# Kernel optimization log

Measured on AMD Instinct MI355X. Metric: run time of the kernel, lower is better.

## Reference

```python
import jax, jax.numpy as jnp
import numpy as np

EMBED_DIM = 1024
NUM_HEADS = 16
HEAD_DIM = EMBED_DIM // NUM_HEADS
EPS = 1e-6
B, T = 4, 8192


def setup_inputs() -> dict:
    key = jax.random.key(0)
    ks = jax.random.split(key, 11)
    s = 1.0 / np.sqrt(EMBED_DIM)
    inp = {
        'query': jax.random.normal(ks[0], (B, T, EMBED_DIM), jnp.float32),
        'key': jax.random.normal(ks[1], (B, T, EMBED_DIM), jnp.float32),
        'value': jax.random.normal(ks[2], (B, T, EMBED_DIM), jnp.float32),
        'Wq': jax.random.normal(ks[3], (EMBED_DIM, EMBED_DIM), jnp.float32) * s,
        'bq': jnp.zeros((EMBED_DIM,), jnp.float32),
        'Wk': jax.random.normal(ks[4], (EMBED_DIM, EMBED_DIM), jnp.float32) * s,
        'bk': jnp.zeros((EMBED_DIM,), jnp.float32),
        'Wv': jax.random.normal(ks[5], (EMBED_DIM, EMBED_DIM), jnp.float32) * s,
        'bv': jnp.zeros((EMBED_DIM,), jnp.float32),
        'Wo': jax.random.normal(ks[6], (EMBED_DIM, EMBED_DIM), jnp.float32) * s,
        'bo': jnp.zeros((EMBED_DIM,), jnp.float32),
    }
    return inp


def _feature_map(x):
    return jax.nn.elu(x) + 1.0


def reference(query, key, value, Wq, bq, Wk, bk, Wv, bv, Wo, bo):
    b, t, _ = query.shape
    # projections (torch Linear: x @ W.T + b)
    q = query @ Wq.T + bq
    k = key @ Wk.T + bk
    v = value @ Wv.T + bv
    # split heads -> (b, h, t, d)
    def split(x):
        return x.reshape(b, t, NUM_HEADS, HEAD_DIM).transpose(0, 2, 1, 3)
    q = _feature_map(split(q))
    k = _feature_map(split(k))
    v = split(v)
    k_sum = k.sum(axis=2)                                   # (b,h,d)
    denom = jnp.einsum('bhtd,bhd->bht', q, k_sum) + EPS     # (b,h,t)
    kv = jnp.einsum('bhtd,bhtv->bhdv', k, v)                # (b,h,d,d)
    out = jnp.einsum('bhtd,bhde->bhte', q, kv) / denom[..., None]
    out = out.transpose(0, 2, 1, 3).reshape(b, t, EMBED_DIM)
    return out @ Wo.T + bo
```

## Files before the change

### kernel.cpp

```cpp
#include <hip/hip_runtime.h>
#include <hip/hip_bf16.h>

typedef long long TLONG;
typedef float  f32x4_t  __attribute__((ext_vector_type(4)));
typedef short  s16x8_t  __attribute__((ext_vector_type(8)));
typedef short  s16x4_t  __attribute__((ext_vector_type(4)));
typedef __bf16 bf16x8_t __attribute__((ext_vector_type(8)));

#define MDIM 32768
#define NDIM 1024
#define KDIM 1024
#define EPSV 1e-6f

#define BARRIER() asm volatile("s_barrier" ::: "memory")
#define SBAR() __builtin_amdgcn_sched_barrier(0)

__device__ __forceinline__ unsigned short f2bf_bits(float f) {
  __hip_bfloat16 h = __float2bfloat16(f);
  return __builtin_bit_cast(unsigned short, h);
}
__device__ __forceinline__ float bf2f(unsigned short u) {
  unsigned int x = ((unsigned int)u) << 16;
  return __builtin_bit_cast(float, x);
}
__device__ __forceinline__ void load_lds16(const void* g, void* l) {
  __builtin_amdgcn_global_load_lds((const __attribute__((address_space(1))) void*)g,
                                   (__attribute__((address_space(3))) void*)l, 16, 0, 0);
}

__device__ __forceinline__ void conv8(const float* __restrict__ in,
                                      unsigned short* __restrict__ out, TLONG i) {
  f32x4_t a = *reinterpret_cast<const f32x4_t*>(in + i);
  f32x4_t b = *reinterpret_cast<const f32x4_t*>(in + i + 4);
  s16x8_t o;
  o[0] = (short)f2bf_bits(a[0]); o[1] = (short)f2bf_bits(a[1]);
  o[2] = (short)f2bf_bits(a[2]); o[3] = (short)f2bf_bits(a[3]);
  o[4] = (short)f2bf_bits(b[0]); o[5] = (short)f2bf_bits(b[1]);
  o[6] = (short)f2bf_bits(b[2]); o[7] = (short)f2bf_bits(b[3]);
  *reinterpret_cast<s16x8_t*>(out + i) = o;
}

__global__ __launch_bounds__(256) void convert3_f32_bf16(
    const float* __restrict__ a, const float* __restrict__ b, const float* __restrict__ c,
    unsigned short* __restrict__ oa, unsigned short* __restrict__ ob,
    unsigned short* __restrict__ oc) {
  int blk = blockIdx.x;
  const float* in; unsigned short* out;
  if (blk < 2048)      { in = a; out = oa; }
  else if (blk < 4096) { in = b; out = ob; blk -= 2048; }
  else                 { in = c; out = oc; blk -= 4096; }
  const TLONG n = 33554432LL;
  TLONG i = ((TLONG)blk * 256 + threadIdx.x) * 8;
  const TLONG stride = 2048LL * 256 * 8;
  for (; i < n; i += stride) conv8(in, out, i);
}
__global__ __launch_bounds__(256) void convertW_f32_bf16(
    const float* __restrict__ a, const float* __restrict__ b, const float* __restrict__ c,
    const float* __restrict__ d, unsigned short* __restrict__ oa,
    unsigned short* __restrict__ ob, unsigned short* __restrict__ oc,
    unsigned short* __restrict__ od) {
  int blk = blockIdx.x;
  const float* in; unsigned short* out;
  if (blk < 512)       { in = a; out = oa; }
  else if (blk < 1024) { in = b; out = ob; blk -= 512; }
  else if (blk < 1536) { in = c; out = oc; blk -= 1024; }
  else                 { in = d; out = od; blk -= 1536; }
  TLONG i = ((TLONG)blk * 256 + threadIdx.x) * 8;
  conv8(in, out, i);
}

template <int FMAP, int OUT>
__global__ __launch_bounds__(512, 2) void gemm256(
    const unsigned short* __restrict__ A, const unsigned short* __restrict__ W,
    const float* __restrict__ bias, void* __restrict__ Cout) {
  __shared__ short lds[65536];
  const int bid = blockIdx.x;
  const int swz = (bid & 7) * 64 + (bid >> 3);
  const int mt = swz >> 2;
  const int nt = swz & 3;

  const int tid = threadIdx.x;
  const int lane = tid & 63;
  const int w = tid >> 6;
  const int wr = w >> 2, wc = w & 3;
  const int l15 = lane & 15, lh = lane >> 4;

  const int arow0 = mt * 256, brow0 = nt * 256;

  auto stage_half = [&](const unsigned short* __restrict__ src, int ldsOff,
                        int grow, int k0) {
#pragma unroll
    for (int i = 0; i < 2; ++i) {
      const int c = i * 512 + tid;
      const int r = c >> 3, ps = c & 7;
      load_lds16(src + (grow + r) * KDIM + k0 + ((ps ^ (r & 7)) * 8),
                 &lds[ldsOff + c * 8]);
    }
  };

  f32x4_t acc[8][4];
#pragma unroll
  for (int m = 0; m < 8; ++m)
#pragma unroll
    for (int n = 0; n < 4; ++n) acc[m][n] = (f32x4_t)0.0f;

  s16x8_t Af[8][2], Bf[4][2];

  auto rdA = [&](int pb, int m, int ks) -> s16x8_t {
    const int row = wr * 128 + m * 16 + l15;
    return *reinterpret_cast<const s16x8_t*>(
        &lds[pb + row * 64 + (((ks * 4 + lh) ^ (row & 7)) * 8)]);
  };
  auto rdB = [&](int pb, int n, int ks) -> s16x8_t {
    const int row = wc * 64 + n * 16 + l15;
    return *reinterpret_cast<const s16x8_t*>(
        &lds[pb + 16384 + row * 64 + (((ks * 4 + lh) ^ (row & 7)) * 8)]);
  };
  auto quad = [&](int mb, int nl) {
    __builtin_amdgcn_s_setprio(1);
#pragma unroll
    for (int m = 0; m < 4; ++m)
#pragma unroll
      for (int n = 0; n < 2; ++n)
#pragma unroll
        for (int ks = 0; ks < 2; ++ks)
          acc[mb + m][nl + n] = __builtin_amdgcn_mfma_f32_16x16x32_bf16(
              __builtin_bit_cast(bf16x8_t, Af[mb + m][ks]),
              __builtin_bit_cast(bf16x8_t, Bf[nl + n][ks]),
              acc[mb + m][nl + n], 0, 0, 0);
    __builtin_amdgcn_s_setprio(0);
  };

  stage_half(A, 0,             arow0,       0);
  stage_half(A, 8192,          arow0 + 128, 0);
  stage_half(W, 16384,         brow0,       0);
  stage_half(W, 16384 + 8192,  brow0 + 128, 0);
  stage_half(A, 32768,         arow0,       64);
  stage_half(A, 32768 + 8192,  arow0 + 128, 64);
  asm volatile("s_waitcnt vmcnt(4)" ::: "memory");
  SBAR();
  BARRIER();

  for (int kt = 0; kt < 16; ++kt) {
    const int p = kt & 1;
    const int pb = p * 32768, qb = 32768 - pb;
    const int k1 = ((kt + 1) & 15) * 64;
    const int k2 = ((kt + 2) & 15) * 64;
#pragma unroll
    for (int m = 0; m < 4; ++m)
#pragma unroll
      for (int ks = 0; ks < 2; ++ks) Af[m][ks] = rdA(pb, m, ks);
#pragma unroll
    for (int n = 0; n < 2; ++n)
#pragma unroll
      for (int ks = 0; ks < 2; ++ks) Bf[n][ks] = rdB(pb, n, ks);
    SBAR();
#pragma unroll
    for (int m = 0; m < 4; ++m)
#pragma unroll
      for (int ks = 0; ks < 2; ++ks) Af[4 + m][ks] = rdA(pb, 4 + m, ks);
    SBAR();
#pragma unroll
    for (int n = 2; n < 4; ++n)
#pragma unroll
      for (int ks = 0; ks < 2; ++ks) Bf[n][ks] = rdB(pb, n, ks);
    SBAR();
    stage_half(W, qb + 16384, brow0, k1);
    BARRIER();
    asm volatile("s_waitcnt lgkmcnt(12)" ::: "memory");
    SBAR();
    quad(0, 0);
    BARRIER();
    stage_half(W, qb + 16384 + 8192, brow0 + 128, k1);
    BARRIER();
    asm volatile("s_waitcnt lgkmcnt(4)" ::: "memory");
    SBAR();
    quad(4, 0);
    BARRIER();
    stage_half(A, pb, arow0, k2);
    BARRIER();
    asm volatile("s_waitcnt lgkmcnt(0)" ::: "memory");
    SBAR();
    quad(0, 2);
    BARRIER();
    stage_half(A, pb + 8192, arow0 + 128, k2);
    BARRIER();
    quad(4, 2);
    asm volatile("s_waitcnt vmcnt(4)" ::: "memory");
    SBAR();
    BARRIER();
  }

#pragma unroll
  for (int n = 0; n < 4; ++n) {
    const int col = nt * 256 + wc * 64 + n * 16 + l15;
    const float bv = bias[col];
#pragma unroll
    for (int m = 0; m < 8; ++m) {
      const int row0 = mt * 256 + wr * 128 + m * 16 + lh * 4;
      if (OUT == 2) {
        const int b = row0 >> 13, tl = row0 & 8191;
        const int h = col >> 6, d = col & 63;
        s16x4_t o;
#pragma unroll
        for (int j = 0; j < 4; ++j) {
          float v = acc[m][n][j] + bv;
          if (FMAP) v = (v > 0.0f) ? (v + 1.0f) : __expf(v);
          o[j] = (short)f2bf_bits(v);
        }
        *reinterpret_cast<s16x4_t*>(
            reinterpret_cast<unsigned short*>(Cout) +
            (((b * 16 + h) * 64 + d) * 8192 + tl)) = o;
      } else {
#pragma unroll
        for (int j = 0; j < 4; ++j) {
          float v = acc[m][n][j] + bv;
          if (FMAP) v = (v > 0.0f) ? (v + 1.0f) : __expf(v);
          if (OUT == 1)
            reinterpret_cast<float*>(Cout)[(row0 + j) * NDIM + col] = v;
          else
            reinterpret_cast<unsigned short*>(Cout)[(row0 + j) * NDIM + col] = f2bf_bits(v);
        }
      }
    }
  }
}

__global__ __launch_bounds__(256) void kv_ksum_mfma(
    const unsigned short* __restrict__ kT, const unsigned short* __restrict__ vT,
    float* __restrict__ kvT, float* __restrict__ ksum) {
  const int bid = blockIdx.x;
  const int bh = bid >> 4, ch = bid & 15;
  const int tid = threadIdx.x;
  const int lane = tid & 63, w = tid >> 6;
  const int l15 = lane & 15, lh = lane >> 4;
  const int dblk = (w >> 1) * 32, eblk = (w & 1) * 32;

  f32x4_t acc[2][2];
#pragma unroll
  for (int m = 0; m < 2; ++m)
#pragma unroll
    for (int n = 0; n < 2; ++n) acc[m][n] = (f32x4_t)0.0f;
  float ks0 = 0.f, ks1 = 0.f;

  const int tbase = ch * 512 + lh * 8;
  const unsigned short* ka = kT + (bh * 64 + dblk + l15) * 8192 + tbase;
  const unsigned short* va = vT + (bh * 64 + eblk + l15) * 8192 + tbase;

  for (int t0 = 0; t0 < 512; t0 += 32) {
    s16x8_t ar[2], br[2];
#pragma unroll
    for (int m = 0; m < 2; ++m)
      ar[m] = *reinterpret_cast<const s16x8_t*>(ka + m * 16 * 8192 + t0);
#pragma unroll
    for (int n = 0; n < 2; ++n)
      br[n] = *reinterpret_cast<const s16x8_t*>(va + n * 16 * 8192 + t0);
#pragma unroll
    for (int m = 0; m < 2; ++m)
#pragma unroll
      for (int n = 0; n < 2; ++n)
        acc[m][n] = __builtin_amdgcn_mfma_f32_16x16x32_bf16(
            __builtin_bit_cast(bf16x8_t, ar[m]),
            __builtin_bit_cast(bf16x8_t, br[n]), acc[m][n], 0, 0, 0);
    if (eblk == 0) {
#pragma unroll
      for (int i = 0; i < 8; ++i) ks0 += bf2f((unsigned short)ar[0][i]);
#pragma unroll
      for (int i = 0; i < 8; ++i) ks1 += bf2f((unsigned short)ar[1][i]);
    }
  }

  if (eblk == 0) {
    ks0 += __shfl_xor(ks0, 16); ks0 += __shfl_xor(ks0, 32);
    ks1 += __shfl_xor(ks1, 16); ks1 += __shfl_xor(ks1, 32);
    if (lh == 0) {
      atomicAdd(&ksum[bh * 64 + dblk + l15], ks0);
      atomicAdd(&ksum[bh * 64 + dblk + 16 + l15], ks1);
    }
  }
#pragma unroll
  for (int n = 0; n < 2; ++n) {
    const int e = eblk + n * 16 + l15;
#pragma unroll
    for (int m = 0; m < 2; ++m) {
      const int d0 = dblk + m * 16 + lh * 4;
#pragma unroll
      for (int j = 0; j < 4; ++j)
        atomicAdd(&kvT[(bh * 64 + e) * 64 + d0 + j], acc[m][n][j]);
    }
  }
}

__global__ __launch_bounds__(256) void attn_apply_kernel(
    const unsigned short* __restrict__ qf, const float* __restrict__ kvT,
    const float* __restrict__ ksum, unsigned short* __restrict__ att) {
  const int bid = blockIdx.x;
  const int swz = (bid & 7) * 256 + (bid >> 3);
  const int bh = swz >> 5;
  const int tile = swz & 31;
  const int b = bh >> 4, h = bh & 15;
  const int tid = threadIdx.x;
  const int lane = tid & 63, w = tid >> 6;
  const int l15 = lane & 15, lh = lane >> 4;

  float ksr[16];
#pragma unroll
  for (int i = 0; i < 16; ++i) ksr[i] = ksum[bh * 64 + lh * 16 + i];

  bf16x8_t bfrag[2][4];
#pragma unroll
  for (int ks2 = 0; ks2 < 2; ++ks2)
#pragma unroll
    for (int n = 0; n < 4; ++n) {
      const float* p = kvT + (bh * 64 + n * 16 + l15) * 64 + ks2 * 32 + lh * 8;
      f32x4_t p0 = *reinterpret_cast<const f32x4_t*>(p);
      f32x4_t p1 = *reinterpret_cast<const f32x4_t*>(p + 4);
      s16x8_t t;
      t[0] = (short)f2bf_bits(p0[0]); t[1] = (short)f2bf_bits(p0[1]);
      t[2] = (short)f2bf_bits(p0[2]); t[3] = (short)f2bf_bits(p0[3]);
      t[4] = (short)f2bf_bits(p1[0]); t[5] = (short)f2bf_bits(p1[1]);
      t[6] = (short)f2bf_bits(p1[2]); t[7] = (short)f2bf_bits(p1[3]);
      bfrag[ks2][n] = __builtin_bit_cast(bf16x8_t, t);
    }

  const int rbase = b * 8192 + tile * 256 + w * 64;
  f32x4_t acc[4][4];
#pragma unroll
  for (int m = 0; m < 4; ++m)
#pragma unroll
    for (int n = 0; n < 4; ++n) acc[m][n] = (f32x4_t)0.0f;
  float rden[4][4];

#pragma unroll
  for (int m = 0; m < 4; ++m) {
    const int row = rbase + m * 16 + l15;
    const unsigned short* qrow = qf + row * 1024 + h * 64;
    bf16x8_t afr[2];
#pragma unroll
    for (int ks2 = 0; ks2 < 2; ++ks2)
      afr[ks2] = __builtin_bit_cast(bf16x8_t,
          *reinterpret_cast<const s16x8_t*>(qrow + ks2 * 32 + lh * 8));
    s16x8_t qa = *reinterpret_cast<const s16x8_t*>(qrow + lh * 16);
    s16x8_t qb = *reinterpret_cast<const s16x8_t*>(qrow + lh * 16 + 8);
    float part = 0.f;
#pragma unroll
    for (int i = 0; i < 8; ++i) part += bf2f((unsigned short)qa[i]) * ksr[i];
#pragma unroll
    for (int i = 0; i < 8; ++i) part += bf2f((unsigned short)qb[i]) * ksr[8 + i];
    part += __shfl_xor(part, 16);
    part += __shfl_xor(part, 32);
#pragma unroll
    for (int j = 0; j < 4; ++j) {
      float dj = __shfl(part, lh * 4 + j);
      rden[m][j] = 1.0f / (dj + EPSV);
    }
#pragma unroll
    for (int ks2 = 0; ks2 < 2; ++ks2)
#pragma unroll
      for (int n = 0; n < 4; ++n)
        acc[m][n] = __builtin_amdgcn_mfma_f32_16x16x32_bf16(afr[ks2], bfrag[ks2][n], acc[m][n], 0, 0, 0);
  }

#pragma unroll
  for (int m = 0; m < 4; ++m)
#pragma unroll
    for (int n = 0; n < 4; ++n) {
      const int col = h * 64 + n * 16 + l15;
#pragma unroll
      for (int j = 0; j < 4; ++j) {
        const int row = rbase + m * 16 + lh * 4 + j;
        att[row * 1024 + col] = f2bf_bits(acc[m][n][j] * rden[m][j]);
      }
    }
}

extern "C" void kernel_launch(void* const* d_in, const int* in_sizes, int n_in,
                              void* d_out, int out_size, void* d_ws, size_t ws_size,
                              hipStream_t stream) {
  const float* query = (const float*)d_in[0];
  const float* key   = (const float*)d_in[1];
  const float* value = (const float*)d_in[2];
  const float* Wq = (const float*)d_in[3];
  const float* bq = (const float*)d_in[4];
  const float* Wk = (const float*)d_in[5];
  const float* bk = (const float*)d_in[6];
  const float* Wv = (const float*)d_in[7];
  const float* bv = (const float*)d_in[8];
  const float* Wo = (const float*)d_in[9];
  const float* bo = (const float*)d_in[10];
  float* out = (float*)d_out;

  if (ws_size < 277889024ULL) return;
  char* ws = (char*)d_ws;
  unsigned short* Vbf = (unsigned short*)(ws + 0);
  unsigned short* qf  = (unsigned short*)(ws + 67108864);
  unsigned short* kTf = (unsigned short*)(ws + 134217728);
  unsigned short* vTf = (unsigned short*)(ws + 201326592);
  unsigned short* Wqb = (unsigned short*)(ws + 268435456);
  unsigned short* Wkb = Wqb + 1048576;
  unsigned short* Wvb = Wkb + 1048576;
  unsigned short* Wob = Wvb + 1048576;
  float* kvT  = (float*)(ws + 276824064);
  float* ksum = (float*)(ws + 277872640);

  unsigned short* Qbf = (unsigned short*)d_out;
  unsigned short* Kbf = Qbf + 33554432;

  hipMemsetAsync(kvT, 0, (size_t)(64 * 64 * 64 + 64 * 64) * sizeof(float), stream);

  convert3_f32_bf16<<<6144, 256, 0, stream>>>(query, key, value, Qbf, Kbf, Vbf);
  convertW_f32_bf16<<<2048, 256, 0, stream>>>(Wq, Wk, Wv, Wo, Wqb, Wkb, Wvb, Wob);

  gemm256<1, 0><<<512, 512, 0, stream>>>(Qbf, Wqb, bq, qf);
  gemm256<1, 2><<<512, 512, 0, stream>>>(Kbf, Wkb, bk, kTf);
  gemm256<0, 2><<<512, 512, 0, stream>>>(Vbf, Wvb, bv, vTf);

  kv_ksum_mfma<<<1024, 256, 0, stream>>>(kTf, vTf, kvT, ksum);

  attn_apply_kernel<<<2048, 256, 0, stream>>>(qf, kvT, ksum, Vbf);

  gemm256<0, 1><<<512, 512, 0, stream>>>(Vbf, Wob, bo, out);
}
```

Baseline: 600.3 us.

## Fuse fp32-to-bf16 activation conversion into projection GEMM A-tile staging

Removes the standalone kernel converting query/key/value to bf16. The projection GEMMs now load fp32 A tiles into registers, convert them and write bf16 into swizzled LDS, with the k-loop reordered to overlap these loads with MFMA work. This avoids writing and re-reading the bf16 activation copies. The cost is losing direct global-to-LDS loads for A, doubling A bytes read per GEMM tile, and more register pressure.

```diff
diff --git a/kernel.cpp b/kernel.cpp
--- a/kernel.cpp
+++ b/kernel.cpp
@@ -28,32 +28,6 @@
                                    (__attribute__((address_space(3))) void*)l, 16, 0, 0);
 }
 
-__device__ __forceinline__ void conv8(const float* __restrict__ in,
-                                      unsigned short* __restrict__ out, TLONG i) {
-  f32x4_t a = *reinterpret_cast<const f32x4_t*>(in + i);
-  f32x4_t b = *reinterpret_cast<const f32x4_t*>(in + i + 4);
-  s16x8_t o;
-  o[0] = (short)f2bf_bits(a[0]); o[1] = (short)f2bf_bits(a[1]);
-  o[2] = (short)f2bf_bits(a[2]); o[3] = (short)f2bf_bits(a[3]);
-  o[4] = (short)f2bf_bits(b[0]); o[5] = (short)f2bf_bits(b[1]);
-  o[6] = (short)f2bf_bits(b[2]); o[7] = (short)f2bf_bits(b[3]);
-  *reinterpret_cast<s16x8_t*>(out + i) = o;
-}
-
-__global__ __launch_bounds__(256) void convert3_f32_bf16(
-    const float* __restrict__ a, const float* __restrict__ b, const float* __restrict__ c,
-    unsigned short* __restrict__ oa, unsigned short* __restrict__ ob,
-    unsigned short* __restrict__ oc) {
-  int blk = blockIdx.x;
-  const float* in; unsigned short* out;
-  if (blk < 2048)      { in = a; out = oa; }
-  else if (blk < 4096) { in = b; out = ob; blk -= 2048; }
-  else                 { in = c; out = oc; blk -= 4096; }
-  const TLONG n = 33554432LL;
-  TLONG i = ((TLONG)blk * 256 + threadIdx.x) * 8;
-  const TLONG stride = 2048LL * 256 * 8;
-  for (; i < n; i += stride) conv8(in, out, i);
-}
 __global__ __launch_bounds__(256) void convertW_f32_bf16(
     const float* __restrict__ a, const float* __restrict__ b, const float* __restrict__ c,
     const float* __restrict__ d, unsigned short* __restrict__ oa,
@@ -66,12 +40,19 @@
   else if (blk < 1536) { in = c; out = oc; blk -= 1024; }
   else                 { in = d; out = od; blk -= 1536; }
   TLONG i = ((TLONG)blk * 256 + threadIdx.x) * 8;
-  conv8(in, out, i);
-}
-
-template <int FMAP, int OUT>
+  f32x4_t x = *reinterpret_cast<const f32x4_t*>(in + i);
+  f32x4_t y = *reinterpret_cast<const f32x4_t*>(in + i + 4);
+  s16x8_t o;
+  o[0] = (short)f2bf_bits(x[0]); o[1] = (short)f2bf_bits(x[1]);
+  o[2] = (short)f2bf_bits(x[2]); o[3] = (short)f2bf_bits(x[3]);
+  o[4] = (short)f2bf_bits(y[0]); o[5] = (short)f2bf_bits(y[1]);
+  o[6] = (short)f2bf_bits(y[2]); o[7] = (short)f2bf_bits(y[3]);
+  *reinterpret_cast<s16x8_t*>(out + i) = o;
+}
+
+template <int FMAP, int OUT, int AF32>
 __global__ __launch_bounds__(512, 2) void gemm256(
-    const unsigned short* __restrict__ A, const unsigned short* __restrict__ W,
+    const void* __restrict__ Ain, const unsigned short* __restrict__ W,
     const float* __restrict__ bias, void* __restrict__ Cout) {
   __shared__ short lds[65536];
   const int bid = blockIdx.x;
@@ -87,8 +68,11 @@
 
   const int arow0 = mt * 256, brow0 = nt * 256;
 
-  auto stage_half = [&](const unsigned short* __restrict__ src, int ldsOff,
-                        int grow, int k0) {
+  const unsigned short* Ab = (const unsigned short*)Ain;
+  const float* Af32 = (const float*)Ain;
+
+  auto stage_half_g = [&](const unsigned short* __restrict__ src, int ldsOff,
+                          int grow, int k0) {
 #pragma unroll
     for (int i = 0; i < 2; ++i) {
       const int c = i * 512 + tid;
@@ -96,6 +80,35 @@
       load_lds16(src + (grow + r) * KDIM + k0 + ((ps ^ (r & 7)) * 8),
                  &lds[ldsOff + c * 8]);
     }
+  };
+
+  f32x4_t Ast[4][2];
+  auto loadA = [&](int k0) {
+#pragma unroll
+    for (int h = 0; h < 2; ++h)
+#pragma unroll
+      for (int i = 0; i < 2; ++i) {
+        const int c = i * 512 + tid;
+        const int r = c >> 3, ps = c & 7;
+        const float* gp = Af32 + (arow0 + h * 128 + r) * KDIM + k0 + ((ps ^ (r & 7)) * 8);
+        Ast[h * 2 + i][0] = *reinterpret_cast<const f32x4_t*>(gp);
+        Ast[h * 2 + i][1] = *reinterpret_cast<const f32x4_t*>(gp + 4);
+      }
+  };
+  auto writeA = [&](int abase) {
+#pragma unroll
+    for (int h = 0; h < 2; ++h)
+#pragma unroll
+      for (int i = 0; i < 2; ++i) {
+        const int c = i * 512 + tid;
+        s16x8_t o;
+#pragma unroll
+        for (int j = 0; j < 4; ++j) {
+          o[j]     = (short)f2bf_bits(Ast[h * 2 + i][0][j]);
+          o[4 + j] = (short)f2bf_bits(Ast[h * 2 + i][1][j]);
+        }
+        *reinterpret_cast<s16x8_t*>(&lds[abase + h * 8192 + c * 8]) = o;
+      }
   };
 
   f32x4_t acc[8][4];
@@ -131,64 +144,133 @@
     __builtin_amdgcn_s_setprio(0);
   };
 
-  stage_half(A, 0,             arow0,       0);
-  stage_half(A, 8192,          arow0 + 128, 0);
-  stage_half(W, 16384,         brow0,       0);
-  stage_half(W, 16384 + 8192,  brow0 + 128, 0);
-  stage_half(A, 32768,         arow0,       64);
-  stage_half(A, 32768 + 8192,  arow0 + 128, 64);
-  asm volatile("s_waitcnt vmcnt(4)" ::: "memory");
-  SBAR();
-  BARRIER();
-
-  for (int kt = 0; kt < 16; ++kt) {
-    const int p = kt & 1;
-    const int pb = p * 32768, qb = 32768 - pb;
-    const int k1 = ((kt + 1) & 15) * 64;
-    const int k2 = ((kt + 2) & 15) * 64;
-#pragma unroll
-    for (int m = 0; m < 4; ++m)
-#pragma unroll
-      for (int ks = 0; ks < 2; ++ks) Af[m][ks] = rdA(pb, m, ks);
-#pragma unroll
-    for (int n = 0; n < 2; ++n)
-#pragma unroll
-      for (int ks = 0; ks < 2; ++ks) Bf[n][ks] = rdB(pb, n, ks);
+  if constexpr (AF32 == 1) {
+    loadA(0);
+    stage_half_g(W, 16384, brow0, 0);
+    stage_half_g(W, 16384 + 8192, brow0 + 128, 0);
+    asm volatile("s_waitcnt vmcnt(4)" ::: "memory");
     SBAR();
-#pragma unroll
-    for (int m = 0; m < 4; ++m)
-#pragma unroll
-      for (int ks = 0; ks < 2; ++ks) Af[4 + m][ks] = rdA(pb, 4 + m, ks);
+    writeA(0);
+    loadA(64);
+    asm volatile("s_waitcnt vmcnt(0)" ::: "memory");
     SBAR();
-#pragma unroll
-    for (int n = 2; n < 4; ++n)
-#pragma unroll
-      for (int ks = 0; ks < 2; ++ks) Bf[n][ks] = rdB(pb, n, ks);
-    SBAR();
-    stage_half(W, qb + 16384, brow0, k1);
-    BARRIER();
-    asm volatile("s_waitcnt lgkmcnt(12)" ::: "memory");
-    SBAR();
-    quad(0, 0);
-    BARRIER();
-    stage_half(W, qb + 16384 + 8192, brow0 + 128, k1);
-    BARRIER();
-    asm volatile("s_waitcnt lgkmcnt(4)" ::: "memory");
-    SBAR();
-    quad(4, 0);
-    BARRIER();
-    stage_half(A, pb, arow0, k2);
-    BARRIER();
+    writeA(32768);
     asm volatile("s_waitcnt lgkmcnt(0)" ::: "memory");
     SBAR();
-    quad(0, 2);
     BARRIER();
-    stage_half(A, pb + 8192, arow0 + 128, k2);
-    BARRIER();
-    quad(4, 2);
+
+    for (int kt = 0; kt < 16; ++kt) {
+      const int p = kt & 1;
+      const int pb = p * 32768, qb = 32768 - pb;
+      const int k1 = ((kt + 1) & 15) * 64;
+      const int k2 = ((kt + 2) & 15) * 64;
+      loadA(k2);
+      SBAR();
+      asm volatile("s_waitcnt vmcnt(8)" ::: "memory");
+      SBAR();
+#pragma unroll
+      for (int m = 0; m < 4; ++m)
+#pragma unroll
+        for (int ks = 0; ks < 2; ++ks) Af[m][ks] = rdA(pb, m, ks);
+#pragma unroll
+      for (int n = 0; n < 2; ++n)
+#pragma unroll
+        for (int ks = 0; ks < 2; ++ks) Bf[n][ks] = rdB(pb, n, ks);
+      SBAR();
+#pragma unroll
+      for (int n = 2; n < 4; ++n)
+#pragma unroll
+        for (int ks = 0; ks < 2; ++ks) Bf[n][ks] = rdB(pb, n, ks);
+      SBAR();
+      stage_half_g(W, qb + 16384, brow0, k1);
+      BARRIER();
+      asm volatile("s_waitcnt lgkmcnt(4)" ::: "memory");
+      SBAR();
+      quad(0, 0);
+      BARRIER();
+      stage_half_g(W, qb + 16384 + 8192, brow0 + 128, k1);
+      BARRIER();
+      asm volatile("s_waitcnt lgkmcnt(0)" ::: "memory");
+      SBAR();
+      quad(0, 2);
+      BARRIER();
+#pragma unroll
+      for (int m = 0; m < 4; ++m)
+#pragma unroll
+        for (int ks = 0; ks < 2; ++ks) Af[4 + m][ks] = rdA(pb, 4 + m, ks);
+      BARRIER();
+      asm volatile("s_waitcnt lgkmcnt(0)" ::: "memory");
+      SBAR();
+      quad(4, 0);
+      BARRIER();
+      asm volatile("s_waitcnt vmcnt(4)" ::: "memory");
+      SBAR();
+      writeA(pb);
+      quad(4, 2);
+      asm volatile("s_waitcnt lgkmcnt(0)" ::: "memory");
+      SBAR();
+      BARRIER();
+    }
+  } else {
+    stage_half_g(Ab, 0,             arow0,       0);
+    stage_half_g(Ab, 8192,          arow0 + 128, 0);
+    stage_half_g(W,  16384,         brow0,       0);
+    stage_half_g(W,  16384 + 8192,  brow0 + 128, 0);
+    stage_half_g(Ab, 32768,         arow0,       64);
+    stage_half_g(Ab, 32768 + 8192,  arow0 + 128, 64);
     asm volatile("s_waitcnt vmcnt(4)" ::: "memory");
     SBAR();
     BARRIER();
+
+    for (int kt = 0; kt < 16; ++kt) {
+      const int p = kt & 1;
+      const int pb = p * 32768, qb = 32768 - pb;
+      const int k1 = ((kt + 1) & 15) * 64;
+      const int k2 = ((kt + 2) & 15) * 64;
+#pragma unroll
+      for (int m = 0; m < 4; ++m)
+#pragma unroll
+        for (int ks = 0; ks < 2; ++ks) Af[m][ks] = rdA(pb, m, ks);
+#pragma unroll
+      for (int n = 0; n < 2; ++n)
+#pragma unroll
+        for (int ks = 0; ks < 2; ++ks) Bf[n][ks] = rdB(pb, n, ks);
+      SBAR();
+#pragma unroll
+      for (int m = 0; m < 4; ++m)
+#pragma unroll
+        for (int ks = 0; ks < 2; ++ks) Af[4 + m][ks] = rdA(pb, 4 + m, ks);
+      SBAR();
+#pragma unroll
+      for (int n = 2; n < 4; ++n)
+#pragma unroll
+        for (int ks = 0; ks < 2; ++ks) Bf[n][ks] = rdB(pb, n, ks);
+      SBAR();
+      stage_half_g(W, qb + 16384, brow0, k1);
+      BARRIER();
+      asm volatile("s_waitcnt lgkmcnt(12)" ::: "memory");
+      SBAR();
+      quad(0, 0);
+      BARRIER();
+      stage_half_g(W, qb + 16384 + 8192, brow0 + 128, k1);
+      BARRIER();
+      asm volatile("s_waitcnt lgkmcnt(4)" ::: "memory");
+      SBAR();
+      quad(4, 0);
+      BARRIER();
+      stage_half_g(Ab, pb, arow0, k2);
+      BARRIER();
+      asm volatile("s_waitcnt lgkmcnt(0)" ::: "memory");
+      SBAR();
+      quad(0, 2);
+      BARRIER();
+      stage_half_g(Ab, pb + 8192, arow0 + 128, k2);
+      BARRIER();
+      quad(4, 2);
+      asm volatile("s_waitcnt vmcnt(4)" ::: "memory");
+      SBAR();
+      BARRIER();
+    }
   }
 
 #pragma unroll
@@ -392,7 +474,7 @@
 
   if (ws_size < 277889024ULL) return;
   char* ws = (char*)d_ws;
-  unsigned short* Vbf = (unsigned short*)(ws + 0);
+  unsigned short* att = (unsigned short*)(ws + 0);
   unsigned short* qf  = (unsigned short*)(ws + 67108864);
   unsigned short* kTf = (unsigned short*)(ws + 134217728);
   unsigned short* vTf = (unsigned short*)(ws + 201326592);
@@ -403,21 +485,17 @@
   float* kvT  = (float*)(ws + 276824064);
   float* ksum = (float*)(ws + 277872640);
 
-  unsigned short* Qbf = (unsigned short*)d_out;
-  unsigned short* Kbf = Qbf + 33554432;
-
   hipMemsetAsync(kvT, 0, (size_t)(64 * 64 * 64 + 64 * 64) * sizeof(float), stream);
 
-  convert3_f32_bf16<<<6144, 256, 0, stream>>>(query, key, value, Qbf, Kbf, Vbf);
   convertW_f32_bf16<<<2048, 256, 0, stream>>>(Wq, Wk, Wv, Wo, Wqb, Wkb, Wvb, Wob);
 
-  gemm256<1, 0><<<512, 512, 0, stream>>>(Qbf, Wqb, bq, qf);
-  gemm256<1, 2><<<512, 512, 0, stream>>>(Kbf, Wkb, bk, kTf);
-  gemm256<0, 2><<<512, 512, 0, stream>>>(Vbf, Wvb, bv, vTf);
+  gemm256<1, 0, 1><<<512, 512, 0, stream>>>(query, Wqb, bq, qf);
+  gemm256<1, 2, 1><<<512, 512, 0, stream>>>(key,   Wkb, bk, kTf);
+  gemm256<0, 2, 1><<<512, 512, 0, stream>>>(value, Wvb, bv, vTf);
 
   kv_ksum_mfma<<<1024, 256, 0, stream>>>(kTf, vTf, kvT, ksum);
 
-  attn_apply_kernel<<<2048, 256, 0, stream>>>(qf, kvT, ksum, Vbf);
-
-  gemm256<0, 1><<<512, 512, 0, stream>>>(Vbf, Wob, bo, out);
-}
+  attn_apply_kernel<<<2048, 256, 0, stream>>>(qf, kvT, ksum, att);
+
+  gemm256<0, 1, 0><<<512, 512, 0, stream>>>(att, Wob, bo, out);
+}
```

Result: faster. 570.8 us (-4.9%).

## Fuse attention apply into output projection GEMM, computing A tiles on the fly

Applied to the files above, without the earlier changes.

Removes the separate attn_apply kernel and its round trip of the attention output through global memory. The output-projection GEMM now builds each head's 128x64 A tile in LDS directly from q, a precomputed bf16 kv matrix and ksum, interleaved with the B-tile prefetch. A small kernel converts kvT to bf16 first, and the input conversion uses nontemporal loads. The tradeoff is that the q-side attention work is redone for each of the four N tiles, the M tile shrinks to 128, and the GEMM main loop grows more complex.

```diff
diff --git a/kernel.cpp b/kernel.cpp
--- a/kernel.cpp
+++ b/kernel.cpp
@@ -30,8 +30,8 @@
 
 __device__ __forceinline__ void conv8(const float* __restrict__ in,
                                       unsigned short* __restrict__ out, TLONG i) {
-  f32x4_t a = *reinterpret_cast<const f32x4_t*>(in + i);
-  f32x4_t b = *reinterpret_cast<const f32x4_t*>(in + i + 4);
+  f32x4_t a = __builtin_nontemporal_load(reinterpret_cast<const f32x4_t*>(in + i));
+  f32x4_t b = __builtin_nontemporal_load(reinterpret_cast<const f32x4_t*>(in + i + 4));
   s16x8_t o;
   o[0] = (short)f2bf_bits(a[0]); o[1] = (short)f2bf_bits(a[1]);
   o[2] = (short)f2bf_bits(a[2]); o[3] = (short)f2bf_bits(a[3]);
@@ -68,6 +68,18 @@
   TLONG i = ((TLONG)blk * 256 + threadIdx.x) * 8;
   conv8(in, out, i);
 }
+__global__ __launch_bounds__(256) void convert_kv(
+    const float* __restrict__ in, unsigned short* __restrict__ out) {
+  TLONG i = ((TLONG)blockIdx.x * 256 + threadIdx.x) * 8;
+  f32x4_t a = *reinterpret_cast<const f32x4_t*>(in + i);
+  f32x4_t b = *reinterpret_cast<const f32x4_t*>(in + i + 4);
+  s16x8_t o;
+  o[0] = (short)f2bf_bits(a[0]); o[1] = (short)f2bf_bits(a[1]);
+  o[2] = (short)f2bf_bits(a[2]); o[3] = (short)f2bf_bits(a[3]);
+  o[4] = (short)f2bf_bits(b[0]); o[5] = (short)f2bf_bits(b[1]);
+  o[6] = (short)f2bf_bits(b[2]); o[7] = (short)f2bf_bits(b[3]);
+  *reinterpret_cast<s16x8_t*>(out + i) = o;
+}
 
 template <int FMAP, int OUT>
 __global__ __launch_bounds__(512, 2) void gemm256(
@@ -216,12 +228,188 @@
         for (int j = 0; j < 4; ++j) {
           float v = acc[m][n][j] + bv;
           if (FMAP) v = (v > 0.0f) ? (v + 1.0f) : __expf(v);
-          if (OUT == 1)
-            reinterpret_cast<float*>(Cout)[(row0 + j) * NDIM + col] = v;
-          else
-            reinterpret_cast<unsigned short*>(Cout)[(row0 + j) * NDIM + col] = f2bf_bits(v);
+          reinterpret_cast<unsigned short*>(Cout)[(row0 + j) * NDIM + col] = f2bf_bits(v);
         }
       }
+    }
+  }
+}
+
+__global__ __launch_bounds__(512, 2) void gemm_out_fused(
+    const unsigned short* __restrict__ qf,
+    const unsigned short* __restrict__ kvbf,
+    const float* __restrict__ ksum,
+    const unsigned short* __restrict__ W,
+    const float* __restrict__ bias, float* __restrict__ out) {
+  __shared__ short lds[49152];
+  const int bid = blockIdx.x;
+  const int swz = (bid & 7) * 128 + (bid >> 3);
+  const int mt = swz >> 2;
+  const int nt = swz & 3;
+
+  const int tid = threadIdx.x;
+  const int lane = tid & 63;
+  const int w = tid >> 6;
+  const int wr = w >> 2, wc = w & 3;
+  const int l15 = lane & 15, lh = lane >> 4;
+
+  const int brow0 = nt * 256;
+  const int row0A = mt * 128;
+  const int bqbase = (mt >> 6) * 16;
+
+  auto stage_halfB = [&](int ldsOff, int grow, int k0) {
+#pragma unroll
+    for (int i = 0; i < 2; ++i) {
+      const int c = i * 512 + tid;
+      const int r = c >> 3, ps = c & 7;
+      load_lds16(W + (grow + r) * KDIM + k0 + ((ps ^ (r & 7)) * 8),
+                 &lds[ldsOff + c * 8]);
+    }
+  };
+
+  auto att_tile = [&](int h, int abase) {
+    const int bh = bqbase + h;
+    const TLONG grow = row0A + w * 16 + l15;
+    const unsigned short* qrow = qf + grow * 1024 + h * 64;
+    s16x8_t afr0 = *reinterpret_cast<const s16x8_t*>(qrow + lh * 8);
+    s16x8_t afr1 = *reinterpret_cast<const s16x8_t*>(qrow + 32 + lh * 8);
+    s16x8_t qa = *reinterpret_cast<const s16x8_t*>(qrow + lh * 16);
+    s16x8_t qb = *reinterpret_cast<const s16x8_t*>(qrow + lh * 16 + 8);
+    s16x8_t bf0[4], bf1[4];
+#pragma unroll
+    for (int n = 0; n < 4; ++n) {
+      const unsigned short* kp = kvbf + ((bh * 64 + n * 16 + l15) * 64) + lh * 8;
+      bf0[n] = *reinterpret_cast<const s16x8_t*>(kp);
+      bf1[n] = *reinterpret_cast<const s16x8_t*>(kp + 32);
+    }
+    const float* ksp = ksum + bh * 64 + lh * 16;
+    f32x4_t ks0 = *reinterpret_cast<const f32x4_t*>(ksp);
+    f32x4_t ks1 = *reinterpret_cast<const f32x4_t*>(ksp + 4);
+    f32x4_t ks2 = *reinterpret_cast<const f32x4_t*>(ksp + 8);
+    f32x4_t ks3 = *reinterpret_cast<const f32x4_t*>(ksp + 12);
+    float part = 0.f;
+#pragma unroll
+    for (int i = 0; i < 4; ++i) {
+      part += bf2f((unsigned short)qa[i]) * ks0[i];
+      part += bf2f((unsigned short)qa[4 + i]) * ks1[i];
+      part += bf2f((unsigned short)qb[i]) * ks2[i];
+      part += bf2f((unsigned short)qb[4 + i]) * ks3[i];
+    }
+    part += __shfl_xor(part, 16);
+    part += __shfl_xor(part, 32);
+    float rden[4];
+#pragma unroll
+    for (int j = 0; j < 4; ++j)
+      rden[j] = 1.0f / (__shfl(part, lh * 4 + j) + EPSV);
+    f32x4_t aacc[4];
+#pragma unroll
+    for (int n = 0; n < 4; ++n) aacc[n] = (f32x4_t)0.0f;
+#pragma unroll
+    for (int n = 0; n < 4; ++n) {
+      aacc[n] = __builtin_amdgcn_mfma_f32_16x16x32_bf16(
+          __builtin_bit_cast(bf16x8_t, afr0), __builtin_bit_cast(bf16x8_t, bf0[n]),
+          aacc[n], 0, 0, 0);
+      aacc[n] = __builtin_amdgcn_mfma_f32_16x16x32_bf16(
+          __builtin_bit_cast(bf16x8_t, afr1), __builtin_bit_cast(bf16x8_t, bf1[n]),
+          aacc[n], 0, 0, 0);
+    }
+#pragma unroll
+    for (int n = 0; n < 4; ++n) {
+      const int col = n * 16 + l15;
+#pragma unroll
+      for (int j = 0; j < 4; ++j) {
+        const int lr = w * 16 + lh * 4 + j;
+        lds[abase + lr * 64 + (((col >> 3) ^ (lr & 7)) * 8) + (col & 7)] =
+            (short)f2bf_bits(aacc[n][j] * rden[j]);
+      }
+    }
+  };
+
+  f32x4_t acc[4][4];
+#pragma unroll
+  for (int m = 0; m < 4; ++m)
+#pragma unroll
+    for (int n = 0; n < 4; ++n) acc[m][n] = (f32x4_t)0.0f;
+
+  s16x8_t Af[4][2], Bf[4][2];
+  auto rdA = [&](int pbA, int m, int ks) -> s16x8_t {
+    const int row = wr * 64 + m * 16 + l15;
+    return *reinterpret_cast<const s16x8_t*>(
+        &lds[pbA + row * 64 + (((ks * 4 + lh) ^ (row & 7)) * 8)]);
+  };
+  auto rdB = [&](int pbB, int n, int ks) -> s16x8_t {
+    const int row = wc * 64 + n * 16 + l15;
+    return *reinterpret_cast<const s16x8_t*>(
+        &lds[pbB + row * 64 + (((ks * 4 + lh) ^ (row & 7)) * 8)]);
+  };
+  auto quad = [&](int nl) {
+    __builtin_amdgcn_s_setprio(1);
+#pragma unroll
+    for (int m = 0; m < 4; ++m)
+#pragma unroll
+      for (int n = 0; n < 2; ++n)
+#pragma unroll
+        for (int ks = 0; ks < 2; ++ks)
+          acc[m][nl + n] = __builtin_amdgcn_mfma_f32_16x16x32_bf16(
+              __builtin_bit_cast(bf16x8_t, Af[m][ks]),
+              __builtin_bit_cast(bf16x8_t, Bf[nl + n][ks]),
+              acc[m][nl + n], 0, 0, 0);
+    __builtin_amdgcn_s_setprio(0);
+  };
+
+  stage_halfB(16384, brow0, 0);
+  stage_halfB(16384 + 8192, brow0 + 128, 0);
+  SBAR();
+  att_tile(0, 0);
+  asm volatile("s_waitcnt lgkmcnt(0)" ::: "memory");
+  SBAR();
+  BARRIER();
+
+  for (int kt = 0; kt < 16; ++kt) {
+    const int p = kt & 1;
+    const int pbA = p * 8192, qbA = 8192 - pbA;
+    const int pbB = 16384 + p * 16384, qbB = 16384 + (1 - p) * 16384;
+    const int h1 = (kt + 1) & 15;
+#pragma unroll
+    for (int m = 0; m < 4; ++m)
+#pragma unroll
+      for (int ks = 0; ks < 2; ++ks) Af[m][ks] = rdA(pbA, m, ks);
+#pragma unroll
+    for (int n = 0; n < 2; ++n)
+#pragma unroll
+      for (int ks = 0; ks < 2; ++ks) Bf[n][ks] = rdB(pbB, n, ks);
+    SBAR();
+#pragma unroll
+    for (int n = 2; n < 4; ++n)
+#pragma unroll
+      for (int ks = 0; ks < 2; ++ks) Bf[n][ks] = rdB(pbB, n, ks);
+    SBAR();
+    stage_halfB(qbB, brow0, h1 * 64);
+    stage_halfB(qbB + 8192, brow0 + 128, h1 * 64);
+    SBAR();
+    asm volatile("s_waitcnt lgkmcnt(4)" ::: "memory");
+    SBAR();
+    quad(0);
+    asm volatile("s_waitcnt lgkmcnt(0)" ::: "memory");
+    SBAR();
+    quad(2);
+    att_tile(h1, qbA);
+    asm volatile("s_waitcnt lgkmcnt(0)" ::: "memory");
+    SBAR();
+    BARRIER();
+  }
+
+#pragma unroll
+  for (int n = 0; n < 4; ++n) {
+    const int col = nt * 256 + wc * 64 + n * 16 + l15;
+    const float bv = bias[col];
+#pragma unroll
+    for (int m = 0; m < 4; ++m) {
+      const int row0 = mt * 128 + wr * 64 + m * 16 + lh * 4;
+#pragma unroll
+      for (int j = 0; j < 4; ++j)
+        __builtin_nontemporal_store(acc[m][n][j] + bv,
+                                    &out[(TLONG)(row0 + j) * NDIM + col]);
     }
   }
 }
@@ -289,89 +477,6 @@
         atomicAdd(&kvT[(bh * 64 + e) * 64 + d0 + j], acc[m][n][j]);
     }
   }
-}
-
-__global__ __launch_bounds__(256) void attn_apply_kernel(
-    const unsigned short* __restrict__ qf, const float* __restrict__ kvT,
-    const float* __restrict__ ksum, unsigned short* __restrict__ att) {
-  const int bid = blockIdx.x;
-  const int swz = (bid & 7) * 256 + (bid >> 3);
-  const int bh = swz >> 5;
-  const int tile = swz & 31;
-  const int b = bh >> 4, h = bh & 15;
-  const int tid = threadIdx.x;
-  const int lane = tid & 63, w = tid >> 6;
-  const int l15 = lane & 15, lh = lane >> 4;
-
-  float ksr[16];
-#pragma unroll
-  for (int i = 0; i < 16; ++i) ksr[i] = ksum[bh * 64 + lh * 16 + i];
-
-  bf16x8_t bfrag[2][4];
-#pragma unroll
-  for (int ks2 = 0; ks2 < 2; ++ks2)
-#pragma unroll
-    for (int n = 0; n < 4; ++n) {
-      const float* p = kvT + (bh * 64 + n * 16 + l15) * 64 + ks2 * 32 + lh * 8;
-      f32x4_t p0 = *reinterpret_cast<const f32x4_t*>(p);
-      f32x4_t p1 = *reinterpret_cast<const f32x4_t*>(p + 4);
-      s16x8_t t;
-      t[0] = (short)f2bf_bits(p0[0]); t[1] = (short)f2bf_bits(p0[1]);
-      t[2] = (short)f2bf_bits(p0[2]); t[3] = (short)f2bf_bits(p0[3]);
-      t[4] = (short)f2bf_bits(p1[0]); t[5] = (short)f2bf_bits(p1[1]);
-      t[6] = (short)f2bf_bits(p1[2]); t[7] = (short)f2bf_bits(p1[3]);
-      bfrag[ks2][n] = __builtin_bit_cast(bf16x8_t, t);
-    }
-
-  const int rbase = b * 8192 + tile * 256 + w * 64;
-  f32x4_t acc[4][4];
-#pragma unroll
-  for (int m = 0; m < 4; ++m)
-#pragma unroll
-    for (int n = 0; n < 4; ++n) acc[m][n] = (f32x4_t)0.0f;
-  float rden[4][4];
-
-#pragma unroll
-  for (int m = 0; m < 4; ++m) {
-    const int row = rbase + m * 16 + l15;
-    const unsigned short* qrow = qf + row * 1024 + h * 64;
-    bf16x8_t afr[2];
-#pragma unroll
-    for (int ks2 = 0; ks2 < 2; ++ks2)
-      afr[ks2] = __builtin_bit_cast(bf16x8_t,
-          *reinterpret_cast<const s16x8_t*>(qrow + ks2 * 32 + lh * 8));
-    s16x8_t qa = *reinterpret_cast<const s16x8_t*>(qrow + lh * 16);
-    s16x8_t qb = *reinterpret_cast<const s16x8_t*>(qrow + lh * 16 + 8);
-    float part = 0.f;
-#pragma unroll
-    for (int i = 0; i < 8; ++i) part += bf2f((unsigned short)qa[i]) * ksr[i];
-#pragma unroll
-    for (int i = 0; i < 8; ++i) part += bf2f((unsigned short)qb[i]) * ksr[8 + i];
-    part += __shfl_xor(part, 16);
-    part += __shfl_xor(part, 32);
-#pragma unroll
-    for (int j = 0; j < 4; ++j) {
-      float dj = __shfl(part, lh * 4 + j);
-      rden[m][j] = 1.0f / (dj + EPSV);
-    }
-#pragma unroll
-    for (int ks2 = 0; ks2 < 2; ++ks2)
-#pragma unroll
-      for (int n = 0; n < 4; ++n)
-        acc[m][n] = __builtin_amdgcn_mfma_f32_16x16x32_bf16(afr[ks2], bfrag[ks2][n], acc[m][n], 0, 0, 0);
-  }
-
-#pragma unroll
-  for (int m = 0; m < 4; ++m)
-#pragma unroll
-    for (int n = 0; n < 4; ++n) {
-      const int col = h * 64 + n * 16 + l15;
-#pragma unroll
-      for (int j = 0; j < 4; ++j) {
-        const int row = rbase + m * 16 + lh * 4 + j;
-        att[row * 1024 + col] = f2bf_bits(acc[m][n][j] * rden[m][j]);
-      }
-    }
 }
 
 extern "C" void kernel_launch(void* const* d_in, const int* in_sizes, int n_in,
@@ -402,6 +507,7 @@
   unsigned short* Wob = Wvb + 1048576;
   float* kvT  = (float*)(ws + 276824064);
   float* ksum = (float*)(ws + 277872640);
+  unsigned short* kvbf = (unsigned short*)(ws + 0);
 
   unsigned short* Qbf = (unsigned short*)d_out;
   unsigned short* Kbf = Qbf + 33554432;
@@ -416,8 +522,7 @@
   gemm256<0, 2><<<512, 512, 0, stream>>>(Vbf, Wvb, bv, vTf);
 
   kv_ksum_mfma<<<1024, 256, 0, stream>>>(kTf, vTf, kvT, ksum);
-
-  attn_apply_kernel<<<2048, 256, 0, stream>>>(qf, kvT, ksum, Vbf);
-
-  gemm256<0, 1><<<512, 512, 0, stream>>>(Vbf, Wob, bo, out);
-}
+  convert_kv<<<128, 256, 0, stream>>>(kvT, kvbf);
+
+  gemm_out_fused<<<1024, 512, 0, stream>>>(qf, kvbf, ksum, Wob, bo, out);
+}
```

New measurement: 739.4 us. +23.2%, slower.
